# Performance work log

Measured on AMD Instinct MI355X. Metric: run time of the kernel, lower is better.

## Reference

```python
import jax, jax.numpy as jnp
import numpy as np


def setup_inputs() -> dict:
    key = jax.random.key(0)
    k1, k2, k3 = jax.random.split(key, 3)
    B, N = 1024, 4096
    kp3d = jax.random.normal(k1, (B, N, 3), dtype=jnp.float32)
    ref_points = jax.random.uniform(k2, (B, N, 2), dtype=jnp.float32)
    weight = jax.random.uniform(k3, (B, N), dtype=jnp.float32)
    return {"kp3d": kp3d, "ref_points": ref_points, "weight": weight}


def reference(kp3d, ref_points, weight):
    # Projected 2D coords (perspective output already applied upstream).
    x = (kp3d[:, :, 0] + 1.0) * 0.5          # [B, N]
    y = 1.0 - (kp3d[:, :, 1] + 1.0) * 0.5    # [B, N]
    z = kp3d[:, :, 2]                         # [B, N]

    # my_normalize: per-batch-row min-max normalization (vectorized).
    # NOTE: result is computed but unused by the loss, exactly as in the
    # original forward (z = my_normalize(z) is dead afterwards).
    z_min = jnp.min(z, axis=1, keepdims=True)
    z_max = jnp.max(z, axis=1, keepdims=True)
    z_norm = (z - z_min) / (z_max - z_min)    # [B, N]

    kp2d = jnp.stack((x, y), axis=2)          # [B, N, 2]

    # kp_loss: weighted per-point 2D Euclidean distance, summed.
    diff = kp2d - ref_points                  # [B, N, 2]
    dist = jnp.sqrt(jnp.sum(diff * diff, axis=2))  # [B, N]
    loss = jnp.sum(weight * dist)
    # z_norm is dead code in the original; loss is the sole output.
    return loss
```

## Files before the change

### kernel.cpp

```cpp
#include <hip/hip_runtime.h>


#define TPB 256

__global__ __launch_bounds__(TPB) void viewpoint_partial_kernel(
    const float* __restrict__ kp3d,
    const float* __restrict__ ref,
    const float* __restrict__ w,
    float* __restrict__ partials,
    int T)
{
    const float4* kp4 = (const float4*)kp3d;
    const float4* rf4 = (const float4*)ref;
    const float4* w4  = (const float4*)w;

    int tid = blockIdx.x * TPB + threadIdx.x;
    int g0 = tid;
    int g1 = tid + T;

    float4 a0 = kp4[3 * g0 + 0];
    float4 a1 = kp4[3 * g0 + 1];
    float4 a2 = kp4[3 * g0 + 2];
    float4 b0 = kp4[3 * g1 + 0];
    float4 b1 = kp4[3 * g1 + 1];
    float4 b2 = kp4[3 * g1 + 2];
    float4 r00 = rf4[2 * g0 + 0];
    float4 r01 = rf4[2 * g0 + 1];
    float4 r10 = rf4[2 * g1 + 0];
    float4 r11 = rf4[2 * g1 + 1];
    float4 w0 = w4[g0];
    float4 w1 = w4[g1];

    float acc = 0.0f;
    float dx, dy;

    dx = fmaf(a0.x, 0.5f, 0.5f) - r00.x;
    dy = fmaf(a0.y, -0.5f, 0.5f) - r00.y;
    acc += w0.x * sqrtf(fmaf(dx, dx, dy * dy));

    dx = fmaf(a0.w, 0.5f, 0.5f) - r00.z;
    dy = fmaf(a1.x, -0.5f, 0.5f) - r00.w;
    acc += w0.y * sqrtf(fmaf(dx, dx, dy * dy));

    dx = fmaf(a1.z, 0.5f, 0.5f) - r01.x;
    dy = fmaf(a1.w, -0.5f, 0.5f) - r01.y;
    acc += w0.z * sqrtf(fmaf(dx, dx, dy * dy));

    dx = fmaf(a2.y, 0.5f, 0.5f) - r01.z;
    dy = fmaf(a2.z, -0.5f, 0.5f) - r01.w;
    acc += w0.w * sqrtf(fmaf(dx, dx, dy * dy));

    dx = fmaf(b0.x, 0.5f, 0.5f) - r10.x;
    dy = fmaf(b0.y, -0.5f, 0.5f) - r10.y;
    acc += w1.x * sqrtf(fmaf(dx, dx, dy * dy));

    dx = fmaf(b0.w, 0.5f, 0.5f) - r10.z;
    dy = fmaf(b1.x, -0.5f, 0.5f) - r10.w;
    acc += w1.y * sqrtf(fmaf(dx, dx, dy * dy));

    dx = fmaf(b1.z, 0.5f, 0.5f) - r11.x;
    dy = fmaf(b1.w, -0.5f, 0.5f) - r11.y;
    acc += w1.z * sqrtf(fmaf(dx, dx, dy * dy));

    dx = fmaf(b2.y, 0.5f, 0.5f) - r11.z;
    dy = fmaf(b2.z, -0.5f, 0.5f) - r11.w;
    acc += w1.w * sqrtf(fmaf(dx, dx, dy * dy));

    #pragma unroll
    for (int off = 32; off > 0; off >>= 1)
        acc += __shfl_down(acc, off, 64);

    __shared__ float wave_sums[TPB / 64];
    int lane = threadIdx.x & 63;
    int wid  = threadIdx.x >> 6;
    if (lane == 0) wave_sums[wid] = acc;
    __syncthreads();

    if (threadIdx.x == 0) {
        partials[blockIdx.x] = wave_sums[0] + wave_sums[1]
                             + wave_sums[2] + wave_sums[3];
    }
}

__global__ __launch_bounds__(256) void final_reduce_kernel(
    const float* __restrict__ partials, float* __restrict__ out, int n)
{
    float acc = 0.0f;
    for (int i = threadIdx.x; i < n; i += 256)
        acc += partials[i];

    #pragma unroll
    for (int off = 32; off > 0; off >>= 1)
        acc += __shfl_down(acc, off, 64);

    __shared__ float wave_sums[4];
    int lane = threadIdx.x & 63;
    int wid  = threadIdx.x >> 6;
    if (lane == 0) wave_sums[wid] = acc;
    __syncthreads();

    if (threadIdx.x == 0)
        out[0] = wave_sums[0] + wave_sums[1] + wave_sums[2] + wave_sums[3];
}

extern "C" void kernel_launch(void* const* d_in, const int* in_sizes, int n_in,
                              void* d_out, int out_size, void* d_ws, size_t ws_size,
                              hipStream_t stream) {
    const float* kp3d = (const float*)d_in[0];
    const float* ref  = (const float*)d_in[1];
    const float* w    = (const float*)d_in[2];
    float* out = (float*)d_out;
    float* partials = (float*)d_ws;

    int npts = in_sizes[2];
    int ngroups = npts / 4;
    int T = ngroups / 2;
    int blocks = T / TPB;

    viewpoint_partial_kernel<<<blocks, TPB, 0, stream>>>(kp3d, ref, w, partials, T);
    final_reduce_kernel<<<1, 256, 0, stream>>>(partials, out, blocks);
}
```

Before: 117.6 us.

## Stage strided float4 loads through LDS for fully coalesced global reads

```diff
diff --git a/kernel.cpp b/kernel.cpp
--- a/kernel.cpp
+++ b/kernel.cpp
@@ -14,22 +14,61 @@
     const float4* rf4 = (const float4*)ref;
     const float4* w4  = (const float4*)w;
 
-    int tid = blockIdx.x * TPB + threadIdx.x;
-    int g0 = tid;
-    int g1 = tid + T;
+    __shared__ float4 lds[3072];
 
-    float4 a0 = kp4[3 * g0 + 0];
-    float4 a1 = kp4[3 * g0 + 1];
-    float4 a2 = kp4[3 * g0 + 2];
-    float4 b0 = kp4[3 * g1 + 0];
-    float4 b1 = kp4[3 * g1 + 1];
-    float4 b2 = kp4[3 * g1 + 2];
-    float4 r00 = rf4[2 * g0 + 0];
-    float4 r01 = rf4[2 * g0 + 1];
-    float4 r10 = rf4[2 * g1 + 0];
-    float4 r11 = rf4[2 * g1 + 1];
-    float4 w0 = w4[g0];
-    float4 w1 = w4[g1];
+    const int t = threadIdx.x;
+
+    const int kpb0 = 768 * blockIdx.x;
+    const int kpb1 = kpb0 + 3 * T;
+    const int rfb0 = 512 * blockIdx.x;
+    const int rfb1 = rfb0 + 2 * T;
+    const int wb0  = 256 * blockIdx.x;
+    const int wb1  = wb0 + T;
+
+    float4 s0  = kp4[kpb0 + t];
+    float4 s1  = kp4[kpb0 + t + 256];
+    float4 s2  = kp4[kpb0 + t + 512];
+    float4 s3  = kp4[kpb1 + t];
+    float4 s4  = kp4[kpb1 + t + 256];
+    float4 s5  = kp4[kpb1 + t + 512];
+    float4 s6  = rf4[rfb0 + t];
+    float4 s7  = rf4[rfb0 + t + 256];
+    float4 s8  = rf4[rfb1 + t];
+    float4 s9  = rf4[rfb1 + t + 256];
+    float4 s10 = w4[wb0 + t];
+    float4 s11 = w4[wb1 + t];
+
+    asm volatile("" ::
+        "v"(s0.x), "v"(s1.x), "v"(s2.x), "v"(s3.x), "v"(s4.x), "v"(s5.x),
+        "v"(s6.x), "v"(s7.x), "v"(s8.x), "v"(s9.x), "v"(s10.x), "v"(s11.x));
+
+    lds[0    + t]       = s0;
+    lds[0    + t + 256] = s1;
+    lds[0    + t + 512] = s2;
+    lds[768  + t]       = s3;
+    lds[768  + t + 256] = s4;
+    lds[768  + t + 512] = s5;
+    lds[1536 + t]       = s6;
+    lds[1536 + t + 256] = s7;
+    lds[2048 + t]       = s8;
+    lds[2048 + t + 256] = s9;
+    lds[2560 + t]       = s10;
+    lds[2816 + t]       = s11;
+
+    __syncthreads();
+
+    float4 a0 = lds[3 * t + 0];
+    float4 a1 = lds[3 * t + 1];
+    float4 a2 = lds[3 * t + 2];
+    float4 b0 = lds[768 + 3 * t + 0];
+    float4 b1 = lds[768 + 3 * t + 1];
+    float4 b2 = lds[768 + 3 * t + 2];
+    float4 r00 = lds[1536 + 2 * t + 0];
+    float4 r01 = lds[1536 + 2 * t + 1];
+    float4 r10 = lds[2048 + 2 * t + 0];
+    float4 r11 = lds[2048 + 2 * t + 1];
+    float4 w0 = lds[2560 + t];
+    float4 w1 = lds[2816 + t];
 
     float acc = 0.0f;
     float dx, dy;
```

Result: slower. 121.6 us (+3.4%).
